# Kernel tuning notes

Hardware: AMD Instinct MI355X
Metric: run time of the kernel (lower is better)

## Reference

```python
import jax, jax.numpy as jnp
import numpy as np

NUM_P = 8192   # number of forward particles
M = 8192       # number of backward smoothing samples
DX = 16        # state dim
DU = 8         # action dim
SIGMA = 1.0    # transition noise std (Gaussian env)


def setup_inputs() -> dict:
    key = jax.random.key(0)
    ks = jax.random.split(key, 7)
    particles = jax.random.normal(ks[0], (NUM_P, DX + DU), dtype=jnp.float32)
    log_weights = jax.random.normal(ks[1], (NUM_P,), dtype=jnp.float32)
    samples_p = jax.random.normal(ks[2], (M, DX), dtype=jnp.float32)
    weights = jax.random.normal(ks[3], (M,), dtype=jnp.float32)
    A = jax.random.normal(ks[4], (DX, DX), dtype=jnp.float32) * 0.1
    B = jax.random.normal(ks[5], (DX, DU), dtype=jnp.float32) * 0.1
    samples_idx = jax.random.randint(ks[6], (NUM_P,), 0, NUM_P)
    return {"particles": particles, "log_weights": log_weights,
            "samples_p": samples_p, "weights": weights,
            "A": A, "B": B, "samples_idx": samples_idx}


def reference(particles, log_weights, samples_p, weights, A, B, samples_idx):
    # backward_smoothing (Doucet et al.): for each backward sample p,
    #   forward_ll = env.log_likelihood(x, u, p)  over all particles
    #   lls = forward_ll - logsumexp(log_weights + forward_ll) + weight
    #   smoothed = logsumexp over samples; log_weights += smoothed
    dx = A.shape[0]
    x = particles[:, :dx]            # [P, DX]
    u = particles[:, dx:]            # [P, DU]
    mu = x @ A.T + u @ B.T           # predicted next state, [P, DX]
    # squared distance via gram trick -> only [M, P] materialized
    sq = (jnp.sum(samples_p * samples_p, axis=1)[:, None]
          + jnp.sum(mu * mu, axis=1)[None, :]
          - 2.0 * samples_p @ mu.T)                      # [M, P]
    log_const = 0.5 * dx * jnp.log(2.0 * jnp.pi * SIGMA * SIGMA)
    forward_ll = -0.5 * sq / (SIGMA * SIGMA) - log_const  # [M, P]
    # per-sample normalization
    norm = jax.scipy.special.logsumexp(log_weights[None, :] + forward_ll, axis=1)  # [M]
    lls = forward_ll - norm[:, None] + weights[:, None]   # [M, P]
    smoothed = jax.scipy.special.logsumexp(lls, axis=0)   # [P]
    new_log_weights = log_weights + smoothed
    return new_log_weights
```

## Files before the change

### kernel.cpp

```cpp
#include <hip/hip_runtime.h>

#define LOG2E 1.44269504088896340736f
#define LN2   0.69314718055994530942f

typedef __attribute__((ext_vector_type(8))) short bf16x8;
typedef __attribute__((ext_vector_type(4))) float f32x4;
typedef __attribute__((ext_vector_type(16))) float f32x16;

#define WS_MUP  0
#define WS_SPT  131072
#define WS_AV1  262144
#define WS_P1   270336
#define WS_P2   794624

__device__ __forceinline__ unsigned short bf16_rne(float x) {
  unsigned int u = __float_as_uint(x);
  u = u + 0x7FFFu + ((u >> 16) & 1u);
  return (unsigned short)(u >> 16);
}
__device__ __forceinline__ float bf16f(unsigned short h) {
  return __uint_as_float(((unsigned int)h) << 16);
}
__device__ __forceinline__ float fast_exp2(float x) {
#if __has_builtin(__builtin_amdgcn_exp2f)
  return __builtin_amdgcn_exp2f(x);
#else
  return exp2f(x);
#endif
}
__device__ __forceinline__ float fast_log2(float x) {
#if __has_builtin(__builtin_amdgcn_logf)
  return __builtin_amdgcn_logf(x);
#else
  return log2f(x);
#endif
}

__device__ __forceinline__ void pack_row(const float* v, unsigned int* buf) {
#pragma unroll
  for (int k = 0; k < 16; k += 2) {
    unsigned short h0 = bf16_rne(v[k]);
    unsigned short h1 = bf16_rne(v[k + 1]);
    float l0 = v[k] - bf16f(h0);
    float l1 = v[k + 1] - bf16f(h1);
    buf[k >> 1] = (unsigned int)h0 | ((unsigned int)h1 << 16);
    buf[8 + (k >> 1)] = (unsigned int)bf16_rne(l0) | ((unsigned int)bf16_rne(l1) << 16);
  }
}

__global__ __launch_bounds__(256) void k_prep(
    const float* __restrict__ particles, const float* __restrict__ lw,
    const float* __restrict__ sp,
    const float* __restrict__ A, const float* __restrict__ B,
    unsigned int* __restrict__ muP, unsigned int* __restrict__ spT,
    float* __restrict__ av1) {
  int j = blockIdx.x * 256 + threadIdx.x;
  float x[24];
  {
    const float4* p4 = (const float4*)(particles + (size_t)j * 24);
#pragma unroll
    for (int q = 0; q < 6; ++q) {
      float4 v = p4[q];
      x[q * 4 + 0] = v.x; x[q * 4 + 1] = v.y; x[q * 4 + 2] = v.z; x[q * 4 + 3] = v.w;
    }
  }
  float mrow[16];
  float m2 = 0.f;
#pragma unroll
  for (int k = 0; k < 16; ++k) {
    float s = 0.f;
#pragma unroll
    for (int l = 0; l < 16; ++l) s += x[l] * A[k * 16 + l];
#pragma unroll
    for (int l = 0; l < 8; ++l) s += x[16 + l] * B[k * 8 + l];
    mrow[k] = s;
    m2 += s * s;
  }
  av1[j] = LOG2E * (lw[j] - 0.5f * m2);

  unsigned int buf[16];
  pack_row(mrow, buf);
  {
    uint4* dst = (uint4*)(muP + (size_t)j * 16);
#pragma unroll
    for (int q = 0; q < 4; ++q)
      dst[q] = make_uint4(buf[q * 4], buf[q * 4 + 1], buf[q * 4 + 2], buf[q * 4 + 3]);
  }
  float srow[16];
  {
    const float4* s4 = (const float4*)(sp + (size_t)j * 16);
#pragma unroll
    for (int q = 0; q < 4; ++q) {
      float4 v = s4[q];
      srow[q * 4 + 0] = LOG2E * v.x; srow[q * 4 + 1] = LOG2E * v.y;
      srow[q * 4 + 2] = LOG2E * v.z; srow[q * 4 + 3] = LOG2E * v.w;
    }
  }
  pack_row(srow, buf);
  {
    uint4* dst = (uint4*)(spT + (size_t)j * 16);
#pragma unroll
    for (int q = 0; q < 4; ++q)
      dst[q] = make_uint4(buf[q * 4], buf[q * 4 + 1], buf[q * 4 + 2], buf[q * 4 + 3]);
  }
}

#define EXPSUM16(d, acc)                                              \
  {                                                                   \
    float e0 = fast_exp2(d[0])  + fast_exp2(d[1]);                    \
    float e1 = fast_exp2(d[2])  + fast_exp2(d[3]);                    \
    float e2 = fast_exp2(d[4])  + fast_exp2(d[5]);                    \
    float e3 = fast_exp2(d[6])  + fast_exp2(d[7]);                    \
    float e4 = fast_exp2(d[8])  + fast_exp2(d[9]);                    \
    float e5 = fast_exp2(d[10]) + fast_exp2(d[11]);                   \
    float e6 = fast_exp2(d[12]) + fast_exp2(d[13]);                   \
    float e7 = fast_exp2(d[14]) + fast_exp2(d[15]);                   \
    acc += ((e0 + e1) + (e2 + e3)) + ((e4 + e5) + (e6 + e7));         \
  }

__global__ __launch_bounds__(256, 4) void k_pass(
    const unsigned int* __restrict__ tilev,
    const unsigned int* __restrict__ statv,
    const float* __restrict__ avv,
    const float* __restrict__ psrc,
    float* __restrict__ part) {
  __shared__ __align__(16) unsigned int tl[128 * 20];
  __shared__ __align__(16) float av_l[128];
  __shared__ float sums[256];
  const int t = threadIdx.x;
  const int chunk = blockIdx.x;
  const int sg    = blockIdx.y;

  {
    const uint4* src = (const uint4*)(tilev + (size_t)chunk * 2048);
#pragma unroll
    for (int q = 0; q < 2; ++q) {
      int f = t + 256 * q;
      int row = f >> 2, s = f & 3;
      *(uint4*)(tl + row * 20 + s * 4) = src[f];
    }
  }

  if (psrc == nullptr) {
    if (t < 128) av_l[t] = avv[chunk * 128 + t];
  } else {
    const int row = t & 127, half = t >> 7;
    float s = 0.f;
    const float* p = psrc + (size_t)(half * 32) * 8192 + chunk * 128 + row;
#pragma unroll 8
    for (int c = 0; c < 32; ++c) s += p[(size_t)c * 8192];
    sums[t] = s;
    __syncthreads();
    if (t < 128) {
      float sv = sums[t] + sums[t + 128];
      av_l[t] = LOG2E * avv[chunk * 128 + t] - fast_log2(sv);
    }
  }
  __syncthreads();

  const int l = t & 63;
  const int wave = t >> 6;
  const int lr = l & 31;
  const int hi = l >> 5;
  const int r0 = sg * 256 + wave * 64;

  const unsigned int* brow0 = statv + (size_t)(r0 + lr) * 16 + hi * 4;
  const unsigned int* brow1 = statv + (size_t)(r0 + 32 + lr) * 16 + hi * 4;
  const bf16x8 b_hi0 = *(const bf16x8*)brow0;
  const bf16x8 b_lo0 = *(const bf16x8*)(brow0 + 8);
  const bf16x8 b_hi1 = *(const bf16x8*)brow1;
  const bf16x8 b_lo1 = *(const bf16x8*)(brow1 + 8);

  float acc0 = 0.f, acc1 = 0.f;
#pragma unroll
  for (int tile = 0; tile < 4; ++tile) {
    const unsigned int* arow = tl + (tile * 32 + lr) * 20 + hi * 4;
    const bf16x8 a_hi = *(const bf16x8*)arow;
    const bf16x8 a_lo = *(const bf16x8*)(arow + 8);

    const f32x4 c0 = *(const f32x4*)(av_l + tile * 32 + 0  + 4 * hi);
    const f32x4 c1 = *(const f32x4*)(av_l + tile * 32 + 8  + 4 * hi);
    const f32x4 c2 = *(const f32x4*)(av_l + tile * 32 + 16 + 4 * hi);
    const f32x4 c3 = *(const f32x4*)(av_l + tile * 32 + 24 + 4 * hi);
    f32x16 d0, d1;
#pragma unroll
    for (int e = 0; e < 4; ++e) {
      d0[e] = c0[e]; d0[4 + e] = c1[e]; d0[8 + e] = c2[e]; d0[12 + e] = c3[e];
      d1[e] = c0[e]; d1[4 + e] = c1[e]; d1[8 + e] = c2[e]; d1[12 + e] = c3[e];
    }
    d0 = __builtin_amdgcn_mfma_f32_32x32x16_bf16(a_hi, b_hi0, d0, 0, 0, 0);
    d0 = __builtin_amdgcn_mfma_f32_32x32x16_bf16(a_lo, b_hi0, d0, 0, 0, 0);
    d0 = __builtin_amdgcn_mfma_f32_32x32x16_bf16(a_hi, b_lo0, d0, 0, 0, 0);
    d1 = __builtin_amdgcn_mfma_f32_32x32x16_bf16(a_hi, b_hi1, d1, 0, 0, 0);
    d1 = __builtin_amdgcn_mfma_f32_32x32x16_bf16(a_lo, b_hi1, d1, 0, 0, 0);
    d1 = __builtin_amdgcn_mfma_f32_32x32x16_bf16(a_hi, b_lo1, d1, 0, 0, 0);

    EXPSUM16(d0, acc0)
    EXPSUM16(d1, acc1)
  }
  acc0 += __shfl_xor(acc0, 32);
  acc1 += __shfl_xor(acc1, 32);
  if (l < 32) part[(size_t)chunk * 8192 + r0 + lr] = acc0;
  else        part[(size_t)chunk * 8192 + r0 + 32 + lr] = acc1;
}

__global__ __launch_bounds__(256) void k_out(
    const float* __restrict__ part, const float* __restrict__ av1,
    float* __restrict__ out) {
  int j = blockIdx.x * 256 + threadIdx.x;
  float s = 0.f;
#pragma unroll
  for (int c = 0; c < 64; ++c) s += part[(size_t)c * 8192 + j];
  out[j] = LN2 * (av1[j] + fast_log2(s));
}

extern "C" void kernel_launch(void* const* d_in, const int* in_sizes, int n_in,
                              void* d_out, int out_size, void* d_ws, size_t ws_size,
                              hipStream_t stream) {
  const float* particles = (const float*)d_in[0];
  const float* lw        = (const float*)d_in[1];
  const float* sp        = (const float*)d_in[2];
  const float* w         = (const float*)d_in[3];
  const float* A         = (const float*)d_in[4];
  const float* B         = (const float*)d_in[5];

  float* ws = (float*)d_ws;
  unsigned int* muP = (unsigned int*)(ws + WS_MUP);
  unsigned int* spT = (unsigned int*)(ws + WS_SPT);
  float* av1  = ws + WS_AV1;
  float* p1   = ws + WS_P1;
  float* p2   = ws + WS_P2;
  float* out  = (float*)d_out;

  k_prep<<<dim3(32), dim3(256), 0, stream>>>(particles, lw, sp, A, B, muP, spT, av1);
  k_pass<<<dim3(64, 32), dim3(256), 0, stream>>>(muP, spT, av1, nullptr, p1);
  k_pass<<<dim3(64, 32), dim3(256), 0, stream>>>(spT, muP, w, p1, p2);
  k_out<<<dim3(32), dim3(256), 0, stream>>>(p2, av1, out);
}
```

Baseline: 47.60 us.

## Factor column bias out of exponent as multiplier and double rows per block

The per-column log-space bias is no longer used to seed the MFMA accumulators. It is exponentiated once per column in shared memory and multiplied in after each exp2, so the MFMAs start from zero and the per-tile accumulator initialisation disappears. Each block now handles two row groups, which halves the grid and amortises the tile load and the column-stat setup across twice the work. The risk is overflow or underflow: exp2 of the bias and the dot product are now computed separately, which could go out of range where the combined exponent would not.

```diff
diff --git a/kernel.cpp b/kernel.cpp
--- a/kernel.cpp
+++ b/kernel.cpp
@@ -105,18 +105,64 @@
   }
 }
 
-#define EXPSUM16(d, acc)                                              \
-  {                                                                   \
-    float e0 = fast_exp2(d[0])  + fast_exp2(d[1]);                    \
-    float e1 = fast_exp2(d[2])  + fast_exp2(d[3]);                    \
-    float e2 = fast_exp2(d[4])  + fast_exp2(d[5]);                    \
-    float e3 = fast_exp2(d[6])  + fast_exp2(d[7]);                    \
-    float e4 = fast_exp2(d[8])  + fast_exp2(d[9]);                    \
-    float e5 = fast_exp2(d[10]) + fast_exp2(d[11]);                   \
-    float e6 = fast_exp2(d[12]) + fast_exp2(d[13]);                   \
-    float e7 = fast_exp2(d[14]) + fast_exp2(d[15]);                   \
-    acc += ((e0 + e1) + (e2 + e3)) + ((e4 + e5) + (e6 + e7));         \
-  }
+#define EXPSUM16W(d, c0, c1, c2, c3, acc)                               \
+  {                                                                     \
+    float m0 = c0[0] * fast_exp2(d[0])  + c0[1] * fast_exp2(d[1]);      \
+    float m1 = c0[2] * fast_exp2(d[2])  + c0[3] * fast_exp2(d[3]);      \
+    float m2 = c1[0] * fast_exp2(d[4])  + c1[1] * fast_exp2(d[5]);      \
+    float m3 = c1[2] * fast_exp2(d[6])  + c1[3] * fast_exp2(d[7]);      \
+    float m4 = c2[0] * fast_exp2(d[8])  + c2[1] * fast_exp2(d[9]);      \
+    float m5 = c2[2] * fast_exp2(d[10]) + c2[3] * fast_exp2(d[11]);     \
+    float m6 = c3[0] * fast_exp2(d[12]) + c3[1] * fast_exp2(d[13]);     \
+    float m7 = c3[2] * fast_exp2(d[14]) + c3[3] * fast_exp2(d[15]);     \
+    acc += ((m0 + m1) + (m2 + m3)) + ((m4 + m5) + (m6 + m7));           \
+  }
+
+__device__ __forceinline__ void inner_pass(
+    const unsigned int* __restrict__ statv, float* __restrict__ part,
+    int chunk, int sg, int t,
+    const unsigned int* __restrict__ tl, const float* __restrict__ eav_l,
+    const f32x16 zc) {
+  const int l = t & 63;
+  const int wave = t >> 6;
+  const int lr = l & 31;
+  const int hi = l >> 5;
+  const int r0 = sg * 256 + wave * 64;
+
+  const unsigned int* brow0 = statv + (size_t)(r0 + lr) * 16 + hi * 4;
+  const unsigned int* brow1 = statv + (size_t)(r0 + 32 + lr) * 16 + hi * 4;
+  const bf16x8 b_hi0 = *(const bf16x8*)brow0;
+  const bf16x8 b_lo0 = *(const bf16x8*)(brow0 + 8);
+  const bf16x8 b_hi1 = *(const bf16x8*)brow1;
+  const bf16x8 b_lo1 = *(const bf16x8*)(brow1 + 8);
+
+  float acc0 = 0.f, acc1 = 0.f;
+#pragma unroll
+  for (int tile = 0; tile < 4; ++tile) {
+    const unsigned int* arow = tl + (tile * 32 + lr) * 20 + hi * 4;
+    const bf16x8 a_hi = *(const bf16x8*)arow;
+    const bf16x8 a_lo = *(const bf16x8*)(arow + 8);
+
+    const f32x4 c0 = *(const f32x4*)(eav_l + tile * 32 + 0  + 4 * hi);
+    const f32x4 c1 = *(const f32x4*)(eav_l + tile * 32 + 8  + 4 * hi);
+    const f32x4 c2 = *(const f32x4*)(eav_l + tile * 32 + 16 + 4 * hi);
+    const f32x4 c3 = *(const f32x4*)(eav_l + tile * 32 + 24 + 4 * hi);
+
+    f32x16 d0 = __builtin_amdgcn_mfma_f32_32x32x16_bf16(a_hi, b_hi0, zc, 0, 0, 0);
+    d0 = __builtin_amdgcn_mfma_f32_32x32x16_bf16(a_lo, b_hi0, d0, 0, 0, 0);
+    d0 = __builtin_amdgcn_mfma_f32_32x32x16_bf16(a_hi, b_lo0, d0, 0, 0, 0);
+    f32x16 d1 = __builtin_amdgcn_mfma_f32_32x32x16_bf16(a_hi, b_hi1, zc, 0, 0, 0);
+    d1 = __builtin_amdgcn_mfma_f32_32x32x16_bf16(a_lo, b_hi1, d1, 0, 0, 0);
+    d1 = __builtin_amdgcn_mfma_f32_32x32x16_bf16(a_hi, b_lo1, d1, 0, 0, 0);
+
+    EXPSUM16W(d0, c0, c1, c2, c3, acc0)
+    EXPSUM16W(d1, c0, c1, c2, c3, acc1)
+  }
+  acc0 += __shfl_xor(acc0, 32);
+  acc1 += __shfl_xor(acc1, 32);
+  if (l < 32) part[(size_t)chunk * 8192 + r0 + lr] = acc0;
+  else        part[(size_t)chunk * 8192 + r0 + 32 + lr] = acc1;
+}
 
 __global__ __launch_bounds__(256, 4) void k_pass(
     const unsigned int* __restrict__ tilev,
@@ -125,11 +171,11 @@
     const float* __restrict__ psrc,
     float* __restrict__ part) {
   __shared__ __align__(16) unsigned int tl[128 * 20];
-  __shared__ __align__(16) float av_l[128];
+  __shared__ __align__(16) float eav_l[128];
   __shared__ float sums[256];
   const int t = threadIdx.x;
   const int chunk = blockIdx.x;
-  const int sg    = blockIdx.y;
+  const int by    = blockIdx.y;
 
   {
     const uint4* src = (const uint4*)(tilev + (size_t)chunk * 2048);
@@ -142,7 +188,7 @@
   }
 
   if (psrc == nullptr) {
-    if (t < 128) av_l[t] = avv[chunk * 128 + t];
+    if (t < 128) eav_l[t] = fast_exp2(avv[chunk * 128 + t]);
   } else {
     const int row = t & 127, half = t >> 7;
     float s = 0.f;
@@ -153,55 +199,15 @@
     __syncthreads();
     if (t < 128) {
       float sv = sums[t] + sums[t + 128];
-      av_l[t] = LOG2E * avv[chunk * 128 + t] - fast_log2(sv);
+      eav_l[t] = fast_exp2(LOG2E * avv[chunk * 128 + t]) / sv;
     }
   }
   __syncthreads();
 
-  const int l = t & 63;
-  const int wave = t >> 6;
-  const int lr = l & 31;
-  const int hi = l >> 5;
-  const int r0 = sg * 256 + wave * 64;
-
-  const unsigned int* brow0 = statv + (size_t)(r0 + lr) * 16 + hi * 4;
-  const unsigned int* brow1 = statv + (size_t)(r0 + 32 + lr) * 16 + hi * 4;
-  const bf16x8 b_hi0 = *(const bf16x8*)brow0;
-  const bf16x8 b_lo0 = *(const bf16x8*)(brow0 + 8);
-  const bf16x8 b_hi1 = *(const bf16x8*)brow1;
-  const bf16x8 b_lo1 = *(const bf16x8*)(brow1 + 8);
-
-  float acc0 = 0.f, acc1 = 0.f;
-#pragma unroll
-  for (int tile = 0; tile < 4; ++tile) {
-    const unsigned int* arow = tl + (tile * 32 + lr) * 20 + hi * 4;
-    const bf16x8 a_hi = *(const bf16x8*)arow;
-    const bf16x8 a_lo = *(const bf16x8*)(arow + 8);
-
-    const f32x4 c0 = *(const f32x4*)(av_l + tile * 32 + 0  + 4 * hi);
-    const f32x4 c1 = *(const f32x4*)(av_l + tile * 32 + 8  + 4 * hi);
-    const f32x4 c2 = *(const f32x4*)(av_l + tile * 32 + 16 + 4 * hi);
-    const f32x4 c3 = *(const f32x4*)(av_l + tile * 32 + 24 + 4 * hi);
-    f32x16 d0, d1;
-#pragma unroll
-    for (int e = 0; e < 4; ++e) {
-      d0[e] = c0[e]; d0[4 + e] = c1[e]; d0[8 + e] = c2[e]; d0[12 + e] = c3[e];
-      d1[e] = c0[e]; d1[4 + e] = c1[e]; d1[8 + e] = c2[e]; d1[12 + e] = c3[e];
-    }
-    d0 = __builtin_amdgcn_mfma_f32_32x32x16_bf16(a_hi, b_hi0, d0, 0, 0, 0);
-    d0 = __builtin_amdgcn_mfma_f32_32x32x16_bf16(a_lo, b_hi0, d0, 0, 0, 0);
-    d0 = __builtin_amdgcn_mfma_f32_32x32x16_bf16(a_hi, b_lo0, d0, 0, 0, 0);
-    d1 = __builtin_amdgcn_mfma_f32_32x32x16_bf16(a_hi, b_hi1, d1, 0, 0, 0);
-    d1 = __builtin_amdgcn_mfma_f32_32x32x16_bf16(a_lo, b_hi1, d1, 0, 0, 0);
-    d1 = __builtin_amdgcn_mfma_f32_32x32x16_bf16(a_hi, b_lo1, d1, 0, 0, 0);
-
-    EXPSUM16(d0, acc0)
-    EXPSUM16(d1, acc1)
-  }
-  acc0 += __shfl_xor(acc0, 32);
-  acc1 += __shfl_xor(acc1, 32);
-  if (l < 32) part[(size_t)chunk * 8192 + r0 + lr] = acc0;
-  else        part[(size_t)chunk * 8192 + r0 + 32 + lr] = acc1;
+  const f32x16 zc = {0.f, 0.f, 0.f, 0.f, 0.f, 0.f, 0.f, 0.f,
+                     0.f, 0.f, 0.f, 0.f, 0.f, 0.f, 0.f, 0.f};
+  inner_pass(statv, part, chunk, by, t, tl, eav_l, zc);
+  inner_pass(statv, part, chunk, by + 16, t, tl, eav_l, zc);
 }
 
 __global__ __launch_bounds__(256) void k_out(
@@ -233,7 +239,7 @@
   float* out  = (float*)d_out;
 
   k_prep<<<dim3(32), dim3(256), 0, stream>>>(particles, lw, sp, A, B, muP, spT, av1);
-  k_pass<<<dim3(64, 32), dim3(256), 0, stream>>>(muP, spT, av1, nullptr, p1);
-  k_pass<<<dim3(64, 32), dim3(256), 0, stream>>>(spT, muP, w, p1, p2);
+  k_pass<<<dim3(64, 16), dim3(256), 0, stream>>>(muP, spT, av1, nullptr, p1);
+  k_pass<<<dim3(64, 16), dim3(256), 0, stream>>>(spT, muP, w, p1, p2);
   k_out<<<dim3(32), dim3(256), 0, stream>>>(p2, av1, out);
 }
```

After: 63.11 us. 32.6% more time.
